# Kernel optimization log

Measured on AMD Instinct MI355X. Metric: run time of the kernel, lower is better.

## Reference

```python
import jax, jax.numpy as jnp
import numpy as np

D_MODEL = 512
N_LAYERS = 4
VOCAB = 256
SEQ = 2048
BATCH = 8
EPS = 1e-5


def _ln(x, g, b):
    mu = jnp.mean(x, axis=-1, keepdims=True)
    var = jnp.mean(jnp.square(x - mu), axis=-1, keepdims=True)
    return (x - mu) * jax.lax.rsqrt(var + EPS) * g + b


def setup_inputs() -> dict:
    key = jax.random.key(0)
    ks = jax.random.split(key, 16)
    d, dff = D_MODEL, 4 * D_MODEL
    s = 0.02
    inp = {
        "tokens": jax.random.randint(ks[0], (BATCH, SEQ), 0, VOCAB, dtype=jnp.int64),
        "emb": jax.random.normal(ks[1], (VOCAB, d), jnp.float32) * s,
        "W_upd": jax.random.normal(ks[2], (d, d), jnp.float32) * s,
        "b_upd": jnp.zeros((d,), jnp.float32),
        "W_f": jax.random.normal(ks[3], (d, d), jnp.float32) * s,
        "b_f": jnp.zeros((d,), jnp.float32),
        "decay_param": jnp.zeros((1,), jnp.float32),
        "norm_g": jnp.ones((d,), jnp.float32),
        "norm_b": jnp.zeros((d,), jnp.float32),
        "cms_ln_g": jnp.ones((N_LAYERS, d), jnp.float32),
        "cms_ln_b": jnp.zeros((N_LAYERS, d), jnp.float32),
        "cms_W1": jax.random.normal(ks[4], (N_LAYERS, d, dff), jnp.float32) * s,
        "cms_b1": jnp.zeros((N_LAYERS, dff), jnp.float32),
        "cms_W2": jax.random.normal(ks[5], (N_LAYERS, dff, d), jnp.float32) * s,
        "cms_b2": jnp.zeros((N_LAYERS, d), jnp.float32),
        "head_W": jax.random.normal(ks[6], (d, VOCAB), jnp.float32) * s,
        "head_b": jnp.zeros((VOCAB,), jnp.float32),
    }
    return inp


def _fast_memory(x, mask, W_upd, b_upd, W_f, b_f, decay_param):
    # x: (B,S,d), mask: (B,S) float
    decay = jax.nn.sigmoid(decay_param[0])
    u = jnp.einsum("bsd,de->bse", x, W_upd) + b_upd  # precompute updates
    u_t = jnp.swapaxes(u, 0, 1)                        # (S,B,d)
    m_t = jnp.swapaxes(mask, 0, 1)[..., None]          # (S,B,1)

    def step(mem, inp):
        u_i, msk = inp
        new = decay * mem + u_i
        mem = msk * new + (1.0 - msk) * mem
        return mem, mem

    mem0 = jnp.zeros((x.shape[0], x.shape[2]), x.dtype)
    _, mems = jax.lax.scan(step, mem0, (u_t, m_t))     # (S,B,d)
    mems = jnp.swapaxes(mems, 0, 1)                    # (B,S,d)
    return jnp.einsum("bsd,de->bse", mems, W_f) + b_f


def reference(tokens, emb, W_upd, b_upd, W_f, b_f, decay_param, norm_g, norm_b,
              cms_ln_g, cms_ln_b, cms_W1, cms_b1, cms_W2, cms_b2, head_W, head_b):
    mask = (tokens != 0).astype(emb.dtype)
    x = emb[tokens]                                    # (B,S,d)
    x = x + _fast_memory(x, mask, W_upd, b_upd, W_f, b_f, decay_param)
    x = _ln(x, norm_g, norm_b)
    for i in range(N_LAYERS):
        h = _ln(x, cms_ln_g[i], cms_ln_b[i])
        h = jax.nn.gelu(jnp.einsum("bsd,df->bsf", h, cms_W1[i]) + cms_b1[i], approximate=False)
        h = jnp.einsum("bsf,fd->bsd", h, cms_W2[i]) + cms_b2[i]
        x = x + h
    return jnp.einsum("bsd,dv->bsv", x, head_W) + head_b
```

## Files before the change

### kernel.cpp

```cpp
#include <hip/hip_runtime.h>
#include <hip/hip_bf16.h>
#include <math.h>

#define D_MODEL 512
#define N_LAYERS 4
#define SEQ 2048
#define BATCH 8
#define M_TOT (BATCH * SEQ)
#define DFF 2048
#define HEAD_V 256
#define SC 32
#define NC (SEQ / SC)

typedef __hip_bfloat16 bf16;
typedef __bf16 bf16x8 __attribute__((ext_vector_type(8)));
typedef float f32x4 __attribute__((ext_vector_type(4)));

__device__ __forceinline__ unsigned short bfbits(float x) {
    bf16 h = __float2bfloat16(x);
    return *(unsigned short*)&h;
}
__device__ __forceinline__ unsigned int pk(float a, float b) {
    return (unsigned int)bfbits(a) | ((unsigned int)bfbits(b) << 16);
}

__global__ void convT_kernel(const float* __restrict__ W, bf16* __restrict__ WT,
                             int R, int C, size_t wstride, size_t tstride) {
    W += (size_t)blockIdx.z * wstride;
    WT += (size_t)blockIdx.z * tstride;
    __shared__ float t[32][33];
    int r0 = blockIdx.x * 32, c0 = blockIdx.y * 32;
    int tx = threadIdx.x, ty = threadIdx.y;
    #pragma unroll
    for (int i = 0; i < 32; i += 8)
        t[ty + i][tx] = W[(size_t)(r0 + ty + i) * C + c0 + tx];
    __syncthreads();
    #pragma unroll
    for (int i = 0; i < 32; i += 8)
        WT[(size_t)(c0 + ty + i) * R + r0 + tx] = __float2bfloat16(t[tx][ty + i]);
}

__global__ void embed_kernel(const int* __restrict__ tokens,
                             const float* __restrict__ emb,
                             float* __restrict__ xf, bf16* __restrict__ xb) {
    int row = blockIdx.x, t = threadIdx.x;
    int tok = tokens[row];
    float4 v = ((const float4*)(emb + (size_t)tok * D_MODEL))[t];
    ((float4*)(xf + (size_t)row * D_MODEL))[t] = v;
    uint2 st; st.x = pk(v.x, v.y); st.y = pk(v.z, v.w);
    ((uint2*)(xb + (size_t)row * D_MODEL))[t] = st;
}

__global__ void scanA_kernel(bf16* __restrict__ u, const int* __restrict__ tokens,
                             const float* __restrict__ decayp,
                             float* __restrict__ L, float* __restrict__ P) {
    int idx = blockIdx.x;
    int dblk = idx & 1;
    int c = (idx >> 1) & (NC - 1);
    int b = idx >> 7;
    int d = dblk * 256 + threadIdx.x;
    float decay = 1.0f / (1.0f + __expf(-decayp[0]));
    const int* tok = tokens + (size_t)b * SEQ + c * SC;
    bf16* up = u + ((size_t)b * SEQ + (size_t)c * SC) * D_MODEL + d;
    float mem = 0.0f;
    #pragma unroll 4
    for (int s = 0; s < SC; ++s) {
        float ui = __bfloat162float(up[(size_t)s * D_MODEL]);
        bool m = (tok[s] != 0);
        mem = (m ? decay : 1.0f) * mem + (m ? ui : 0.0f);
        up[(size_t)s * D_MODEL] = __float2bfloat16(mem);
    }
    L[((size_t)b * NC + c) * D_MODEL + d] = mem;
    if (threadIdx.x == 0 && dblk == 0) {
        int cnt = 0;
        for (int s = 0; s < SC; ++s) cnt += (tok[s] != 0);
        P[b * NC + c] = __powf(decay, (float)cnt);
    }
}

__global__ void scanB_kernel(const float* __restrict__ L, const float* __restrict__ P,
                             float* __restrict__ Mc) {
    int b = blockIdx.x >> 1;
    int d = (blockIdx.x & 1) * 256 + threadIdx.x;
    float carry = 0.0f;
    for (int c = 0; c < NC; ++c) {
        size_t off = ((size_t)b * NC + c) * D_MODEL + d;
        Mc[off] = carry;
        carry = P[b * NC + c] * carry + L[off];
    }
}

__global__ void scanC_kernel(bf16* __restrict__ u, const int* __restrict__ tokens,
                             const float* __restrict__ decayp,
                             const float* __restrict__ Mc) {
    int idx = blockIdx.x;
    int dblk = idx & 1;
    int c = (idx >> 1) & (NC - 1);
    int b = idx >> 7;
    if (c == 0) return;
    int d = dblk * 256 + threadIdx.x;
    float decay = 1.0f / (1.0f + __expf(-decayp[0]));
    const int* tok = tokens + (size_t)b * SEQ + c * SC;
    bf16* up = u + ((size_t)b * SEQ + (size_t)c * SC) * D_MODEL + d;
    float carry = Mc[((size_t)b * NC + c) * D_MODEL + d];
    float coeff = 1.0f;
    #pragma unroll 4
    for (int s = 0; s < SC; ++s) {
        bool m = (tok[s] != 0);
        coeff *= (m ? decay : 1.0f);
        float local = __bfloat162float(up[(size_t)s * D_MODEL]);
        up[(size_t)s * D_MODEL] = __float2bfloat16(local + carry * coeff);
    }
}

__device__ __forceinline__ void ln_body(const float* __restrict__ in,
                                        float* __restrict__ outf,
                                        bf16* __restrict__ outb,
                                        const float* __restrict__ g,
                                        const float* __restrict__ b,
                                        int WF, int WB) {
    int w = threadIdx.x >> 6, lane = threadIdx.x & 63;
    int row = blockIdx.x * 4 + w;
    const float4* ip = (const float4*)(in + (size_t)row * D_MODEL);
    float4 v0 = ip[lane * 2], v1 = ip[lane * 2 + 1];
    float s1 = v0.x + v0.y + v0.z + v0.w + v1.x + v1.y + v1.z + v1.w;
    float s2 = v0.x * v0.x + v0.y * v0.y + v0.z * v0.z + v0.w * v0.w +
               v1.x * v1.x + v1.y * v1.y + v1.z * v1.z + v1.w * v1.w;
    #pragma unroll
    for (int off = 32; off; off >>= 1) {
        s1 += __shfl_xor(s1, off);
        s2 += __shfl_xor(s2, off);
    }
    float mu = s1 * (1.0f / D_MODEL);
    float var = s2 * (1.0f / D_MODEL) - mu * mu;
    float rstd = rsqrtf(var + 1e-5f);
    const float4* g4 = (const float4*)g;
    const float4* b4 = (const float4*)b;
    float4 g0 = g4[lane * 2], g1 = g4[lane * 2 + 1];
    float4 b0 = b4[lane * 2], b1 = b4[lane * 2 + 1];
    float4 o0, o1;
    o0.x = (v0.x - mu) * rstd * g0.x + b0.x;
    o0.y = (v0.y - mu) * rstd * g0.y + b0.y;
    o0.z = (v0.z - mu) * rstd * g0.z + b0.z;
    o0.w = (v0.w - mu) * rstd * g0.w + b0.w;
    o1.x = (v1.x - mu) * rstd * g1.x + b1.x;
    o1.y = (v1.y - mu) * rstd * g1.y + b1.y;
    o1.z = (v1.z - mu) * rstd * g1.z + b1.z;
    o1.w = (v1.w - mu) * rstd * g1.w + b1.w;
    if (WF) {
        float4* op = (float4*)(outf + (size_t)row * D_MODEL);
        op[lane * 2] = o0; op[lane * 2 + 1] = o1;
    }
    if (WB) {
        uint4 st;
        st.x = pk(o0.x, o0.y); st.y = pk(o0.z, o0.w);
        st.z = pk(o1.x, o1.y); st.w = pk(o1.z, o1.w);
        ((uint4*)(outb + (size_t)row * D_MODEL))[lane] = st;
    }
}

__global__ void ln_f32_kernel(const float* __restrict__ in, float* __restrict__ outf,
                              const float* __restrict__ g, const float* __restrict__ b) {
    ln_body(in, outf, nullptr, g, b, 1, 0);
}
__global__ void ln_b16_kernel(const float* __restrict__ in, bf16* __restrict__ outb,
                              const float* __restrict__ g, const float* __restrict__ b) {
    ln_body(in, nullptr, outb, g, b, 0, 1);
}

#define STAGE(s, k0)                                                          \
    do {                                                                      \
        _Pragma("unroll")                                                     \
        for (int it = 0; it < 2; ++it) {                                      \
            int c = tid + it * 256;                                           \
            int p = c * 16;                                                   \
            int l = p ^ (((p >> 7) & 7) << 4);                                \
            __builtin_amdgcn_global_load_lds(                                 \
                A + (size_t)(m0 + (l >> 6)) * K + (k0) + ((l & 63) >> 1),     \
                smem + (s) * ABYTES + (c & ~63) * 16, 16, 0, 0);              \
        }                                                                     \
        _Pragma("unroll")                                                     \
        for (int it = 0; it < LB; ++it) {                                     \
            int c = tid + it * 256;                                           \
            int p = c * 16;                                                   \
            int l = p ^ (((p >> 7) & 7) << 4);                                \
            __builtin_amdgcn_global_load_lds(                                 \
                BT + (size_t)(n0 + (l >> 6)) * K + (k0) + ((l & 63) >> 1),    \
                smem + 2 * ABYTES + (s) * BBYTES + (c & ~63) * 16, 16, 0, 0); \
        }                                                                     \
    } while (0)

template <int BN, int GELU, int RES, int OBF>
__device__ __forceinline__ void gemm_body(char* smem,
                          const bf16* __restrict__ A, const bf16* __restrict__ BT,
                          const float* __restrict__ bias, const float* __restrict__ R,
                          float* __restrict__ Cf, bf16* __restrict__ Cb,
                          int N, int K) {
    constexpr int NJ = BN / 32;
    constexpr int LB = BN / 64;
    constexpr int ABYTES = 128 * 32 * 2;
    constexpr int BBYTES = BN * 32 * 2;
    constexpr int ST = 16 * NJ + 4;
    const int tid = threadIdx.x;
    const int lane = tid & 63;
    const int w = tid >> 6, wr = w >> 1, wc = w & 1;
    const int lm = lane & 15, lk = lane >> 4;
    const int sw = ((lm >> 1) & 7) << 4;
    const int m0 = blockIdx.x * 128, n0 = blockIdx.y * BN;

    f32x4 acc[4][NJ] = {};

    const int nt = K / 32;
    STAGE(0, 0);
    asm volatile("s_waitcnt vmcnt(0)" ::: "memory");
    __builtin_amdgcn_s_barrier();
    __builtin_amdgcn_sched_barrier(0);
    int cur = 0;
    for (int t = 0; t < nt; ++t) {
        if (t + 1 < nt) STAGE(cur ^ 1, (t + 1) * 32);
        const char* Asc = smem + cur * ABYTES;
        const char* Bsc = smem + 2 * ABYTES + cur * BBYTES;
        bf16x8 fa[4], fb[NJ];
        #pragma unroll
        for (int i = 0; i < 4; ++i) {
            int la = (wr * 64 + i * 16 + lm) * 64 + lk * 16;
            fa[i] = *(const bf16x8*)(Asc + (la ^ sw));
        }
        #pragma unroll
        for (int j = 0; j < NJ; ++j) {
            int lb = (wc * (BN / 2) + j * 16 + lm) * 64 + lk * 16;
            fb[j] = *(const bf16x8*)(Bsc + (lb ^ sw));
        }
        #pragma unroll
        for (int i = 0; i < 4; ++i)
            #pragma unroll
            for (int j = 0; j < NJ; ++j)
                acc[i][j] = __builtin_amdgcn_mfma_f32_16x16x32_bf16(fa[i], fb[j], acc[i][j], 0, 0, 0);
        asm volatile("s_waitcnt vmcnt(0)" ::: "memory");
        __builtin_amdgcn_s_barrier();
        __builtin_amdgcn_sched_barrier(0);
        cur ^= 1;
    }

    float* ep = (float*)smem + w * 16 * ST;
    const int r2 = lane >> 2;
    const int q = lane & 3;
    constexpr int CW = 16 * NJ;
    const int gc0 = n0 + wc * CW + q * 4 * NJ;
    #pragma unroll
    for (int i = 0; i < 4; ++i) {
        #pragma unroll
        for (int j = 0; j < NJ; ++j)
            #pragma unroll
            for (int r = 0; r < 4; ++r)
                ep[(lk * 4 + r) * ST + j * 16 + lm] = acc[i][j][r];
        int grow = m0 + wr * 64 + i * 16 + r2;
        float4 fx[NJ];
        #pragma unroll
        for (int v = 0; v < NJ; ++v)
            fx[v] = *(const float4*)&ep[r2 * ST + q * 4 * NJ + v * 4];
        #pragma unroll
        for (int v = 0; v < NJ; ++v) {
            float4 bb = *(const float4*)(bias + gc0 + v * 4);
            fx[v].x += bb.x; fx[v].y += bb.y; fx[v].z += bb.z; fx[v].w += bb.w;
            if (GELU) {
                fx[v].x = 0.5f * fx[v].x * (1.0f + erff(fx[v].x * 0.70710678118654752f));
                fx[v].y = 0.5f * fx[v].y * (1.0f + erff(fx[v].y * 0.70710678118654752f));
                fx[v].z = 0.5f * fx[v].z * (1.0f + erff(fx[v].z * 0.70710678118654752f));
                fx[v].w = 0.5f * fx[v].w * (1.0f + erff(fx[v].w * 0.70710678118654752f));
            }
            if (RES) {
                float4 rr = *(const float4*)(R + (size_t)grow * N + gc0 + v * 4);
                fx[v].x += rr.x; fx[v].y += rr.y; fx[v].z += rr.z; fx[v].w += rr.w;
            }
        }
        if (OBF == 0 || OBF == 2) {
            #pragma unroll
            for (int v = 0; v < NJ; ++v)
                *(float4*)(Cf + (size_t)grow * N + gc0 + v * 4) = fx[v];
        }
        if (OBF >= 1) {
            #pragma unroll
            for (int v = 0; v < NJ; v += 2) {
                uint4 st;
                st.x = pk(fx[v].x, fx[v].y);
                st.y = pk(fx[v].z, fx[v].w);
                st.z = pk(fx[v + 1].x, fx[v + 1].y);
                st.w = pk(fx[v + 1].z, fx[v + 1].w);
                *(uint4*)(Cb + (size_t)grow * N + gc0 + v * 4) = st;
            }
        }
    }
}

#define DEF_GEMM(name, BN, GELU, RES, OBF)                                    \
__launch_bounds__(256) __global__ void name(                                  \
        const bf16* __restrict__ A, const bf16* __restrict__ BT,              \
        const float* __restrict__ bias, const float* __restrict__ R,          \
        float* __restrict__ Cf, bf16* __restrict__ Cb, int N, int K) {        \
    __shared__ char smem[16384 + (BN) * 128];                                 \
    gemm_body<BN, GELU, RES, OBF>(smem, A, BT, bias, R, Cf, Cb, N, K);        \
}

DEF_GEMM(gemm_u,       128, 0, 0, 1)
DEF_GEMM(gemm_res,     128, 0, 1, 0)
DEF_GEMM(gemm_gelu,    128, 1, 0, 1)
DEF_GEMM(gemm_resboth, 128, 0, 1, 2)
DEF_GEMM(gemm_plain,   128, 0, 0, 0)
DEF_GEMM(gemm64_res,      64, 0, 1, 0)
DEF_GEMM(gemm64_resboth,  64, 0, 1, 2)

extern "C" void kernel_launch(void* const* d_in, const int* in_sizes, int n_in,
                              void* d_out, int out_size, void* d_ws, size_t ws_size,
                              hipStream_t stream) {
    const int*   tokens = (const int*)d_in[0];
    const float* emb    = (const float*)d_in[1];
    const float* W_upd  = (const float*)d_in[2];
    const float* b_upd  = (const float*)d_in[3];
    const float* W_f    = (const float*)d_in[4];
    const float* b_f    = (const float*)d_in[5];
    const float* decayp = (const float*)d_in[6];
    const float* norm_g = (const float*)d_in[7];
    const float* norm_b = (const float*)d_in[8];
    const float* cms_g  = (const float*)d_in[9];
    const float* cms_b  = (const float*)d_in[10];
    const float* cW1    = (const float*)d_in[11];
    const float* cb1    = (const float*)d_in[12];
    const float* cW2    = (const float*)d_in[13];
    const float* cb2    = (const float*)d_in[14];
    const float* head_W = (const float*)d_in[15];
    const float* head_b = (const float*)d_in[16];
    float* out = (float*)d_out;

    const int M = M_TOT, D = D_MODEL, F = DFF, V = HEAD_V;

    float* xf = (float*)d_ws;
    bf16*  lnb = (bf16*)((char*)d_ws + (size_t)M * D * 4);
    bf16*  wb  = (bf16*)((char*)lnb + (size_t)M * D * 2);
    const size_t WB_ELEMS = 9043968;
    char* dyn = (char*)wb + WB_ELEMS * 2;
    size_t used = (size_t)(dyn - (char*)d_ws);
    size_t avail = ws_size > used ? ws_size - used : 0;
    int MC = 4096;
    if (avail >= (size_t)16384 * F * 2) MC = 16384;
    else if (avail >= (size_t)8192 * F * 2) MC = 8192;
    bf16* ub = (bf16*)dyn;
    bf16* hb = (bf16*)dyn;

    float* scanL = out;
    float* scanM = out + (size_t)BATCH * NC * D;
    float* scanP = scanM + (size_t)BATCH * NC * D;

    bf16* WupdT = wb;
    bf16* WfT   = wb + 262144;
    bf16* W1T   = wb + 524288;
    bf16* W2T   = wb + 4718592;
    bf16* HWT   = wb + 8912896;

    dim3 tb(32, 8);
    convT_kernel<<<dim3(16, 16, 2), tb, 0, stream>>>(W_upd, WupdT, D, D,
                                                     (size_t)(W_f - W_upd), 262144);
    convT_kernel<<<dim3(16, 64, N_LAYERS), tb, 0, stream>>>(cW1, W1T, D, F,
                                                            (size_t)D * F, 1048576);
    convT_kernel<<<dim3(64, 16, N_LAYERS), tb, 0, stream>>>(cW2, W2T, F, D,
                                                            (size_t)F * D, 1048576);
    convT_kernel<<<dim3(16, 8, 1), tb, 0, stream>>>(head_W, HWT, D, V, 0, 0);

    embed_kernel<<<M, 128, 0, stream>>>(tokens, emb, xf, lnb);

    gemm_u<<<dim3(M / 128, D / 128), 256, 0, stream>>>(
        lnb, WupdT, b_upd, nullptr, nullptr, ub, D, D);
    scanA_kernel<<<BATCH * NC * 2, 256, 0, stream>>>(ub, tokens, decayp, scanL, scanP);
    scanB_kernel<<<BATCH * 2, 256, 0, stream>>>(scanL, scanP, scanM);
    scanC_kernel<<<BATCH * NC * 2, 256, 0, stream>>>(ub, tokens, decayp, scanM);
    gemm_res<<<dim3(M / 128, D / 128), 256, 0, stream>>>(
        ub, WfT, b_f, xf, xf, nullptr, D, D);
    ln_f32_kernel<<<M / 4, 256, 0, stream>>>(xf, xf, norm_g, norm_b);

    for (int l = 0; l < N_LAYERS; ++l) {
        ln_b16_kernel<<<M / 4, 256, 0, stream>>>(xf, lnb,
                                                 cms_g + (size_t)l * D,
                                                 cms_b + (size_t)l * D);
        bool last = (l == N_LAYERS - 1);
        for (int mc = 0; mc < M; mc += MC) {
            gemm_gelu<<<dim3(MC / 128, F / 128), 256, 0, stream>>>(
                lnb + (size_t)mc * D, W1T + (size_t)l * 1048576,
                cb1 + (size_t)l * F, nullptr, nullptr, hb, F, D);
            if (MC >= 8192) {
                if (last)
                    gemm_resboth<<<dim3(MC / 128, D / 128), 256, 0, stream>>>(
                        hb, W2T + (size_t)l * 1048576, cb2 + (size_t)l * D,
                        xf + (size_t)mc * D, xf + (size_t)mc * D,
                        lnb + (size_t)mc * D, D, F);
                else
                    gemm_res<<<dim3(MC / 128, D / 128), 256, 0, stream>>>(
                        hb, W2T + (size_t)l * 1048576, cb2 + (size_t)l * D,
                        xf + (size_t)mc * D, xf + (size_t)mc * D, nullptr, D, F);
            } else {
                if (last)
                    gemm64_resboth<<<dim3(MC / 128, D / 64), 256, 0, stream>>>(
                        hb, W2T + (size_t)l * 1048576, cb2 + (size_t)l * D,
                        xf + (size_t)mc * D, xf + (size_t)mc * D,
                        lnb + (size_t)mc * D, D, F);
                else
                    gemm64_res<<<dim3(MC / 128, D / 64), 256, 0, stream>>>(
                        hb, W2T + (size_t)l * 1048576, cb2 + (size_t)l * D,
                        xf + (size_t)mc * D, xf + (size_t)mc * D, nullptr, D, F);
            }
        }
    }

    gemm_plain<<<dim3(M / 128, V / 128), 256, 0, stream>>>(
        lnb, HWT, head_b, nullptr, out, nullptr, V, D);
}
```

Baseline: 591.1 us.

## Enlarge GEMM M-tile to 256 rows and use tanh-approx GELU

```diff
diff --git a/kernel.cpp b/kernel.cpp
--- a/kernel.cpp
+++ b/kernel.cpp
@@ -22,6 +22,12 @@
 }
 __device__ __forceinline__ unsigned int pk(float a, float b) {
     return (unsigned int)bfbits(a) | ((unsigned int)bfbits(b) << 16);
+}
+
+__device__ __forceinline__ float gelu_f(float x) {
+    float t2 = 1.5957691216f * (x + 0.044715f * x * x * x);
+    float e = __expf(t2);
+    return x - x * __builtin_amdgcn_rcpf(e + 1.0f);
 }
 
 __global__ void convT_kernel(const float* __restrict__ W, bf16* __restrict__ WT,
@@ -171,7 +177,7 @@
 #define STAGE(s, k0)                                                          \
     do {                                                                      \
         _Pragma("unroll")                                                     \
-        for (int it = 0; it < 2; ++it) {                                      \
+        for (int it = 0; it < 4; ++it) {                                      \
             int c = tid + it * 256;                                           \
             int p = c * 16;                                                   \
             int l = p ^ (((p >> 7) & 7) << 4);                                \
@@ -197,8 +203,9 @@
                           float* __restrict__ Cf, bf16* __restrict__ Cb,
                           int N, int K) {
     constexpr int NJ = BN / 32;
+    constexpr int MI = 8;
     constexpr int LB = BN / 64;
-    constexpr int ABYTES = 128 * 32 * 2;
+    constexpr int ABYTES = 256 * 32 * 2;
     constexpr int BBYTES = BN * 32 * 2;
     constexpr int ST = 16 * NJ + 4;
     const int tid = threadIdx.x;
@@ -206,9 +213,9 @@
     const int w = tid >> 6, wr = w >> 1, wc = w & 1;
     const int lm = lane & 15, lk = lane >> 4;
     const int sw = ((lm >> 1) & 7) << 4;
-    const int m0 = blockIdx.x * 128, n0 = blockIdx.y * BN;
-
-    f32x4 acc[4][NJ] = {};
+    const int m0 = blockIdx.x * 256, n0 = blockIdx.y * BN;
+
+    f32x4 acc[MI][NJ] = {};
 
     const int nt = K / 32;
     STAGE(0, 0);
@@ -220,10 +227,10 @@
         if (t + 1 < nt) STAGE(cur ^ 1, (t + 1) * 32);
         const char* Asc = smem + cur * ABYTES;
         const char* Bsc = smem + 2 * ABYTES + cur * BBYTES;
-        bf16x8 fa[4], fb[NJ];
-        #pragma unroll
-        for (int i = 0; i < 4; ++i) {
-            int la = (wr * 64 + i * 16 + lm) * 64 + lk * 16;
+        bf16x8 fa[MI], fb[NJ];
+        #pragma unroll
+        for (int i = 0; i < MI; ++i) {
+            int la = (wr * 128 + i * 16 + lm) * 64 + lk * 16;
             fa[i] = *(const bf16x8*)(Asc + (la ^ sw));
         }
         #pragma unroll
@@ -232,7 +239,7 @@
             fb[j] = *(const bf16x8*)(Bsc + (lb ^ sw));
         }
         #pragma unroll
-        for (int i = 0; i < 4; ++i)
+        for (int i = 0; i < MI; ++i)
             #pragma unroll
             for (int j = 0; j < NJ; ++j)
                 acc[i][j] = __builtin_amdgcn_mfma_f32_16x16x32_bf16(fa[i], fb[j], acc[i][j], 0, 0, 0);
@@ -248,13 +255,13 @@
     constexpr int CW = 16 * NJ;
     const int gc0 = n0 + wc * CW + q * 4 * NJ;
     #pragma unroll
-    for (int i = 0; i < 4; ++i) {
+    for (int i = 0; i < MI; ++i) {
         #pragma unroll
         for (int j = 0; j < NJ; ++j)
             #pragma unroll
             for (int r = 0; r < 4; ++r)
                 ep[(lk * 4 + r) * ST + j * 16 + lm] = acc[i][j][r];
-        int grow = m0 + wr * 64 + i * 16 + r2;
+        int grow = m0 + wr * 128 + i * 16 + r2;
         float4 fx[NJ];
         #pragma unroll
         for (int v = 0; v < NJ; ++v)
@@ -264,10 +271,10 @@
             float4 bb = *(const float4*)(bias + gc0 + v * 4);
             fx[v].x += bb.x; fx[v].y += bb.y; fx[v].z += bb.z; fx[v].w += bb.w;
             if (GELU) {
-                fx[v].x = 0.5f * fx[v].x * (1.0f + erff(fx[v].x * 0.70710678118654752f));
-                fx[v].y = 0.5f * fx[v].y * (1.0f + erff(fx[v].y * 0.70710678118654752f));
-                fx[v].z = 0.5f * fx[v].z * (1.0f + erff(fx[v].z * 0.70710678118654752f));
-                fx[v].w = 0.5f * fx[v].w * (1.0f + erff(fx[v].w * 0.70710678118654752f));
+                fx[v].x = gelu_f(fx[v].x);
+                fx[v].y = gelu_f(fx[v].y);
+                fx[v].z = gelu_f(fx[v].z);
+                fx[v].w = gelu_f(fx[v].w);
             }
             if (RES) {
                 float4 rr = *(const float4*)(R + (size_t)grow * N + gc0 + v * 4);
@@ -294,11 +301,11 @@
 }
 
 #define DEF_GEMM(name, BN, GELU, RES, OBF)                                    \
-__launch_bounds__(256) __global__ void name(                                  \
+__launch_bounds__(256, 2) __global__ void name(                               \
         const bf16* __restrict__ A, const bf16* __restrict__ BT,              \
         const float* __restrict__ bias, const float* __restrict__ R,          \
         float* __restrict__ Cf, bf16* __restrict__ Cb, int N, int K) {        \
-    __shared__ char smem[16384 + (BN) * 128];                                 \
+    __shared__ char smem[2 * 16384 + 2 * (BN) * 64];                          \
     gemm_body<BN, GELU, RES, OBF>(smem, A, BT, bias, R, Cf, Cb, N, K);        \
 }
 
@@ -306,9 +313,7 @@
 DEF_GEMM(gemm_res,     128, 0, 1, 0)
 DEF_GEMM(gemm_gelu,    128, 1, 0, 1)
 DEF_GEMM(gemm_resboth, 128, 0, 1, 2)
-DEF_GEMM(gemm_plain,   128, 0, 0, 0)
-DEF_GEMM(gemm64_res,      64, 0, 1, 0)
-DEF_GEMM(gemm64_resboth,  64, 0, 1, 2)
+DEF_GEMM(gemm64_plain,  64, 0, 0, 0)
 
 extern "C" void kernel_launch(void* const* d_in, const int* in_sizes, int n_in,
                               void* d_out, int out_size, void* d_ws, size_t ws_size,
@@ -368,12 +373,12 @@
 
     embed_kernel<<<M, 128, 0, stream>>>(tokens, emb, xf, lnb);
 
-    gemm_u<<<dim3(M / 128, D / 128), 256, 0, stream>>>(
+    gemm_u<<<dim3(M / 256, D / 128), 256, 0, stream>>>(
         lnb, WupdT, b_upd, nullptr, nullptr, ub, D, D);
     scanA_kernel<<<BATCH * NC * 2, 256, 0, stream>>>(ub, tokens, decayp, scanL, scanP);
     scanB_kernel<<<BATCH * 2, 256, 0, stream>>>(scanL, scanP, scanM);
     scanC_kernel<<<BATCH * NC * 2, 256, 0, stream>>>(ub, tokens, decayp, scanM);
-    gemm_res<<<dim3(M / 128, D / 128), 256, 0, stream>>>(
+    gemm_res<<<dim3(M / 256, D / 128), 256, 0, stream>>>(
         ub, WfT, b_f, xf, xf, nullptr, D, D);
     ln_f32_kernel<<<M / 4, 256, 0, stream>>>(xf, xf, norm_g, norm_b);
 
@@ -383,33 +388,21 @@
                                                  cms_b + (size_t)l * D);
         bool last = (l == N_LAYERS - 1);
         for (int mc = 0; mc < M; mc += MC) {
-            gemm_gelu<<<dim3(MC / 128, F / 128), 256, 0, stream>>>(
+            gemm_gelu<<<dim3(MC / 256, F / 128), 256, 0, stream>>>(
                 lnb + (size_t)mc * D, W1T + (size_t)l * 1048576,
                 cb1 + (size_t)l * F, nullptr, nullptr, hb, F, D);
-            if (MC >= 8192) {
-                if (last)
-                    gemm_resboth<<<dim3(MC / 128, D / 128), 256, 0, stream>>>(
-                        hb, W2T + (size_t)l * 1048576, cb2 + (size_t)l * D,
-                        xf + (size_t)mc * D, xf + (size_t)mc * D,
-                        lnb + (size_t)mc * D, D, F);
-                else
-                    gemm_res<<<dim3(MC / 128, D / 128), 256, 0, stream>>>(
-                        hb, W2T + (size_t)l * 1048576, cb2 + (size_t)l * D,
-                        xf + (size_t)mc * D, xf + (size_t)mc * D, nullptr, D, F);
-            } else {
-                if (last)
-                    gemm64_resboth<<<dim3(MC / 128, D / 64), 256, 0, stream>>>(
-                        hb, W2T + (size_t)l * 1048576, cb2 + (size_t)l * D,
-                        xf + (size_t)mc * D, xf + (size_t)mc * D,
-                        lnb + (size_t)mc * D, D, F);
-                else
-                    gemm64_res<<<dim3(MC / 128, D / 64), 256, 0, stream>>>(
-                        hb, W2T + (size_t)l * 1048576, cb2 + (size_t)l * D,
-                        xf + (size_t)mc * D, xf + (size_t)mc * D, nullptr, D, F);
-            }
-        }
-    }
-
-    gemm_plain<<<dim3(M / 128, V / 128), 256, 0, stream>>>(
+            if (last)
+                gemm_resboth<<<dim3(MC / 256, D / 128), 256, 0, stream>>>(
+                    hb, W2T + (size_t)l * 1048576, cb2 + (size_t)l * D,
+                    xf + (size_t)mc * D, xf + (size_t)mc * D,
+                    lnb + (size_t)mc * D, D, F);
+            else
+                gemm_res<<<dim3(MC / 256, D / 128), 256, 0, stream>>>(
+                    hb, W2T + (size_t)l * 1048576, cb2 + (size_t)l * D,
+                    xf + (size_t)mc * D, xf + (size_t)mc * D, nullptr, D, F);
+        }
+    }
+
+    gemm64_plain<<<dim3(M / 256, V / 64), 256, 0, stream>>>(
         lnb, HWT, head_b, nullptr, out, nullptr, V, D);
 }
```

New measurement: 607.5 us. 2.8% more time.
